# Performance work log

Measured on AMD Instinct MI355X. Metric: run time of the kernel, lower is better.

## Reference

```python
import jax, jax.numpy as jnp
import numpy as np

N, D, DFF, H, L = 98280, 192, 384, 8, 36
S = N // L  # 2730 sets per partition
HD = D // H
EPS = 1e-5


def _ln(x, g, b):
    m = x.mean(-1, keepdims=True)
    v = ((x - m) ** 2).mean(-1, keepdims=True)
    return (x - m) * jax.lax.rsqrt(v + EPS) * g + b


def _mha(q, k, v, Wqkv, bqkv, Wo, bo, mask):
    # q,k,v: (S, L, D); mask: (S, L), True = padded key
    Wq, Wk, Wv = jnp.split(Wqkv, 3, axis=0)
    bq, bk, bv = jnp.split(bqkv, 3)
    qh = (q @ Wq.T + bq).reshape(S, L, H, HD)
    kh = (k @ Wk.T + bk).reshape(S, L, H, HD)
    vh = (v @ Wv.T + bv).reshape(S, L, H, HD)
    scores = jnp.einsum('slhd,smhd->shlm', qh, kh) / np.sqrt(HD).astype(np.float32)
    scores = jnp.where(mask[:, None, None, :], -1e9, scores)
    attn = jax.nn.softmax(scores, axis=-1)
    out = jnp.einsum('shlm,smhd->slhd', attn, vh).reshape(S, L, D)
    return out @ Wo.T + bo


def _layer(x, pos, inds, mask, Wqkv, bqkv, Wo, bo, W1, b1, W2, b2,
           g1, be1, g2, be2, gn, bn):
    identity = x
    sf = x[inds]                 # gather voxels into sets: (S, L, D)
    qk = sf + pos[inds]          # pos added to q and k only (value = sf)
    src2 = _mha(qk, qk, sf, Wqkv, bqkv, Wo, bo, mask)
    flat = inds.reshape(-1)
    # torch.unique(return_inverse) + flip + scatter == take FIRST occurrence
    # of each voxel id; .at[].min is deterministic under duplicates.
    perm = jnp.full((N,), flat.shape[0], jnp.int32).at[flat].min(
        jnp.arange(flat.shape[0], dtype=jnp.int32))
    src2 = src2.reshape(-1, D)[perm]   # scatter back: (N, D)
    x = _ln(x + src2, g1, be1)
    ff = jnp.maximum(x @ W1.T + b1, 0.0) @ W2.T + b2
    x = _ln(x + ff, g2, be2)
    return _ln(x + identity, gn, bn)   # DSVT_EncoderLayer residual norm


def reference(src, inds0, inds1, mask0, mask1, pos0, pos1,
              Wqkv, bqkv, Wo, bo, W1, b1, W2, b2,
              g1, be1, g2, be2, gn, bn, block_id):
    inds = (inds0, inds1)
    masks = (mask0, mask1)
    pos = (pos0, pos1)
    out = src
    for i in range(2):  # two set partitions within the shift (shift_id = block_id % 2)
        out = _layer(out, pos[i], inds[i], masks[i],
                     Wqkv[i], bqkv[i], Wo[i], bo[i],
                     W1[i], b1[i], W2[i], b2[i],
                     g1[i], be1[i], g2[i], be2[i], gn[i], bn[i])
    return out


def setup_inputs():
    key = jax.random.key(0)
    ks = jax.random.split(key, 16)
    sd = 0.02
    return {
        "src": jax.random.normal(ks[0], (N, D), jnp.float32),
        "inds0": jax.random.permutation(ks[1], N).reshape(S, L).astype(jnp.int32),
        "inds1": jax.random.permutation(ks[2], N).reshape(S, L).astype(jnp.int32),
        "mask0": jnp.zeros((S, L), bool),
        "mask1": jnp.zeros((S, L), bool),
        "pos0": jax.random.normal(ks[3], (N, D), jnp.float32),
        "pos1": jax.random.normal(ks[4], (N, D), jnp.float32),
        "Wqkv": sd * jax.random.normal(ks[5], (2, 3 * D, D), jnp.float32),
        "bqkv": jnp.zeros((2, 3 * D), jnp.float32),
        "Wo": sd * jax.random.normal(ks[6], (2, D, D), jnp.float32),
        "bo": jnp.zeros((2, D), jnp.float32),
        "W1": sd * jax.random.normal(ks[7], (2, DFF, D), jnp.float32),
        "b1": jnp.zeros((2, DFF), jnp.float32),
        "W2": sd * jax.random.normal(ks[8], (2, D, DFF), jnp.float32),
        "b2": jnp.zeros((2, D), jnp.float32),
        "g1": jnp.ones((2, D), jnp.float32),
        "be1": jnp.zeros((2, D), jnp.float32),
        "g2": jnp.ones((2, D), jnp.float32),
        "be2": jnp.zeros((2, D), jnp.float32),
        "gn": jnp.ones((2, D), jnp.float32),
        "bn": jnp.zeros((2, D), jnp.float32),
        "block_id": 0,
    }
```

## Files before the change

### kernel.cpp

```cpp
#include <hip/hip_runtime.h>
#include <stdint.h>

#define NVOX   98280
#define S_SETS 2730
#define L_SET  36
#define D_MODEL 192
#define D_FF    384
#define N_HEADS 8
#define H_DIM   24

using s16x8 = __attribute__((ext_vector_type(8))) short;
using s16x4 = __attribute__((ext_vector_type(4))) short;
using f32x4 = __attribute__((ext_vector_type(4))) float;

__device__ __forceinline__ float bf2f(unsigned short h) {
    unsigned u = ((unsigned)h) << 16;
    return __builtin_bit_cast(float, u);
}
__device__ __forceinline__ unsigned short f2bf(float f) {
    unsigned u = __builtin_bit_cast(unsigned, f);
    u += 0x7FFF + ((u >> 16) & 1);
    return (unsigned short)(u >> 16);
}

__global__ __launch_bounds__(256)
void convert_f32_bf16(const float* __restrict__ src, short* __restrict__ dst, int n)
{
    int i = blockIdx.x * 256 + threadIdx.x;
    if (i < n) dst[i] = (short)f2bf(src[i]);
}

__global__ __launch_bounds__(256)
void gather_kernel(const float* __restrict__ x, const float* __restrict__ pos,
                   const int* __restrict__ inds,
                   short* __restrict__ qk, short* __restrict__ sf)
{
    int f = blockIdx.x * 4 + (threadIdx.x >> 6);
    int lane = threadIdx.x & 63;
    if (lane >= 48) return;
    int v = inds[f];
    float4 a = *(const float4*)(x + (size_t)v * D_MODEL + lane * 4);
    float4 p = *(const float4*)(pos + (size_t)v * D_MODEL + lane * 4);
    s16x4 q, s;
    q[0] = (short)f2bf(a.x + p.x); q[1] = (short)f2bf(a.y + p.y);
    q[2] = (short)f2bf(a.z + p.z); q[3] = (short)f2bf(a.w + p.w);
    s[0] = (short)f2bf(a.x); s[1] = (short)f2bf(a.y);
    s[2] = (short)f2bf(a.z); s[3] = (short)f2bf(a.w);
    *(s16x4*)(qk + (size_t)f * D_MODEL + lane * 4) = q;
    *(s16x4*)(sf + (size_t)f * D_MODEL + lane * 4) = s;
}

__global__ __launch_bounds__(512, 4)
void qkv_direct(const short* __restrict__ qk, const short* __restrict__ sf,
                const short* __restrict__ W, const float* __restrict__ bias,
                short* __restrict__ C, int n)
{
    __shared__ char Bs[36864];
    const int bx = blockIdx.x;
    const int sec = bx >> 1, half = bx & 1;
    const int colOff = sec * 192 + half * 96;
    const short* Ap = (sec == 2) ? sf : qk;
    const short* Wp = W + (size_t)colOff * 192;
    const int rowBase = blockIdx.y * 128;
    const int tid = threadIdx.x;

    #pragma unroll
    for (int t = tid; t < 2304; t += 512) {
        int row = t / 24, c8 = t % 24;
        s16x8 v = *(const s16x8*)(Wp + (size_t)row * 192 + c8 * 8);
        *(s16x8*)(Bs + row * 384 + ((c8 * 16) ^ ((row & 7) << 4))) = v;
    }
    __syncthreads();

    const int wid = tid >> 6, lane = tid & 63;
    const int lr = lane & 15, kb = lane >> 4;
    const int arow = rowBase + wid * 16 + lr;
    const bool rv = arow < n;
    const short* Arow = Ap + (size_t)arow * 192 + kb * 8;

    f32x4 acc[6] = {};
    #pragma unroll
    for (int ks = 0; ks < 6; ++ks) {
        s16x8 a = {};
        if (rv) a = *(const s16x8*)(Arow + ks * 32);
        s16x8 b[6];
        #pragma unroll
        for (int fj = 0; fj < 6; ++fj) {
            int row = fj * 16 + lr;
            b[fj] = *(const s16x8*)(Bs + row * 384 + ((ks * 64 + kb * 16) ^ ((row & 7) << 4)));
        }
        #pragma unroll
        for (int fj = 0; fj < 6; ++fj)
            acc[fj] = __builtin_amdgcn_mfma_f32_16x16x32_bf16(a, b[fj], acc[fj], 0, 0, 0);
    }
    #pragma unroll
    for (int fj = 0; fj < 6; ++fj) {
        int col = colOff + fj * 16 + lr;
        float bv = bias[col];
        #pragma unroll
        for (int r = 0; r < 4; ++r) {
            int grow = rowBase + wid * 16 + kb * 4 + r;
            if (grow < n)
                C[(size_t)grow * 576 + col] = (short)f2bf(acc[fj][r] + bv);
        }
    }
}

__global__ __launch_bounds__(512)
void attn_set_kernel(const short* __restrict__ qkv, const unsigned char* __restrict__ mask,
                     short* __restrict__ attn_out)
{
    const int s = blockIdx.x;
    __shared__ float KV[2][L_SET][200];
    __shared__ int msk[L_SET];
    const int tid = threadIdx.x;
    const int wid = tid >> 6;
    const int lane = tid & 63;

    for (int t = tid; t < 1728; t += 512) {
        int w = t >= 864;
        int u = t - (w ? 864 : 0);
        int l = u / 24, c8 = u % 24;
        s16x8 v = *(const s16x8*)(qkv + (size_t)(s * L_SET + l) * 576 + 192 + w * 192 + c8 * 8);
        #pragma unroll
        for (int e = 0; e < 8; ++e) KV[w][l][c8 * 8 + e] = bf2f((unsigned short)v[e]);
    }
    if (tid < L_SET) msk[tid] = mask[(size_t)s * L_SET + tid];
    __syncthreads();

    if (lane < L_SET) {
        float q[H_DIM];
        size_t qb = (size_t)(s * L_SET + lane) * 576 + wid * H_DIM;
        #pragma unroll
        for (int j = 0; j < 3; ++j) {
            s16x8 t8 = *(const s16x8*)(qkv + qb + j * 8);
            #pragma unroll
            for (int e = 0; e < 8; ++e) q[j * 8 + e] = bf2f((unsigned short)t8[e]);
        }
        float sc[L_SET];
        float mx = -1e30f;
        #pragma unroll
        for (int m = 0; m < L_SET; ++m) {
            float a = 0.f;
            #pragma unroll
            for (int j = 0; j < 6; ++j) {
                float4 k4 = *(const float4*)&KV[0][m][wid * H_DIM + j * 4];
                a = fmaf(q[j*4+0], k4.x, a); a = fmaf(q[j*4+1], k4.y, a);
                a = fmaf(q[j*4+2], k4.z, a); a = fmaf(q[j*4+3], k4.w, a);
            }
            a *= 0.20412414523193154f;
            if (msk[m] != 0) a = -1e9f;
            sc[m] = a;
            mx = fmaxf(mx, a);
        }
        float ssum = 0.f;
        #pragma unroll
        for (int m = 0; m < L_SET; ++m) { float e = __expf(sc[m] - mx); sc[m] = e; ssum += e; }
        const float rinv = 1.f / ssum;
        float o[H_DIM];
        #pragma unroll
        for (int d = 0; d < H_DIM; ++d) o[d] = 0.f;
        #pragma unroll
        for (int m = 0; m < L_SET; ++m) {
            float p = sc[m] * rinv;
            #pragma unroll
            for (int j = 0; j < 6; ++j) {
                float4 v4 = *(const float4*)&KV[1][m][wid * H_DIM + j * 4];
                o[j*4+0] = fmaf(p, v4.x, o[j*4+0]); o[j*4+1] = fmaf(p, v4.y, o[j*4+1]);
                o[j*4+2] = fmaf(p, v4.z, o[j*4+2]); o[j*4+3] = fmaf(p, v4.w, o[j*4+3]);
            }
        }
        size_t ob = (size_t)(s * L_SET + lane) * D_MODEL + wid * H_DIM;
        #pragma unroll
        for (int j = 0; j < 3; ++j) {
            s16x8 t8;
            #pragma unroll
            for (int e = 0; e < 8; ++e) t8[e] = (short)f2bf(o[j * 8 + e]);
            *(s16x8*)(attn_out + ob + j * 8) = t8;
        }
    }
}

__device__ __forceinline__ float wave_sum64(float v) {
    #pragma unroll
    for (int off = 32; off > 0; off >>= 1) v += __shfl_xor(v, off, 64);
    return v;
}

__global__ __launch_bounds__(512)
void wo_ln1(const short* __restrict__ attnb, const short* __restrict__ Wo,
            const float* __restrict__ bo, const int* __restrict__ inds,
            const float* __restrict__ xin,
            const float* __restrict__ g1, const float* __restrict__ be1,
            short* __restrict__ x1, int n)
{
    extern __shared__ char pool[];
    char* As = pool;
    char* Bs = pool + 49152;
    float* Cf = (float*)pool;
    const int rowBase = blockIdx.x * 128;
    const int tid = threadIdx.x;

    #pragma unroll
    for (int t = tid; t < 3072; t += 512) {
        int row = t / 24, c8 = t % 24;
        int grow = rowBase + row;
        s16x8 v = {};
        if (grow < n) v = *(const s16x8*)(attnb + (size_t)grow * 192 + c8 * 8);
        *(s16x8*)(As + row * 384 + ((c8 * 16) ^ ((row & 7) << 4))) = v;
    }
    #pragma unroll
    for (int t = tid; t < 4608; t += 512) {
        int row = t / 24, c8 = t % 24;
        s16x8 v = *(const s16x8*)(Wo + (size_t)row * 192 + c8 * 8);
        *(s16x8*)(Bs + row * 384 + ((c8 * 16) ^ ((row & 7) << 4))) = v;
    }
    __syncthreads();

    const int wid = tid >> 6, lane = tid & 63;
    const int lr = lane & 15, kb = lane >> 4;
    const int wm = wid & 3, wn = wid >> 2;
    f32x4 acc[2][6] = {};
    #pragma unroll
    for (int ks = 0; ks < 6; ++ks) {
        s16x8 a[2], b[6];
        #pragma unroll
        for (int fi = 0; fi < 2; ++fi) {
            int row = wm * 32 + fi * 16 + lr;
            a[fi] = *(const s16x8*)(As + row * 384 + ((ks * 64 + kb * 16) ^ ((row & 7) << 4)));
        }
        #pragma unroll
        for (int fj = 0; fj < 6; ++fj) {
            int row = wn * 96 + fj * 16 + lr;
            b[fj] = *(const s16x8*)(Bs + row * 384 + ((ks * 64 + kb * 16) ^ ((row & 7) << 4)));
        }
        #pragma unroll
        for (int fi = 0; fi < 2; ++fi)
            #pragma unroll
            for (int fj = 0; fj < 6; ++fj)
                acc[fi][fj] = __builtin_amdgcn_mfma_f32_16x16x32_bf16(a[fi], b[fj], acc[fi][fj], 0, 0, 0);
    }
    __syncthreads();
    #pragma unroll
    for (int fj = 0; fj < 6; ++fj) {
        int col = wn * 96 + fj * 16 + lr;
        float bv = bo[col];
        #pragma unroll
        for (int fi = 0; fi < 2; ++fi)
            #pragma unroll
            for (int r = 0; r < 4; ++r) {
                int row = wm * 32 + fi * 16 + kb * 4 + r;
                Cf[row * 192 + col] = acc[fi][fj][r] + bv;
            }
    }
    __syncthreads();

    int vv[16];
    #pragma unroll
    for (int i = 0; i < 16; ++i) {
        int f = rowBase + wid * 16 + i;
        vv[i] = (f < n) ? inds[f] : 0;
    }
    float4 xr[16];
    #pragma unroll
    for (int i = 0; i < 16; ++i)
        xr[i] = (lane < 48) ? *(const float4*)(xin + (size_t)vv[i] * D_MODEL + lane * 4)
                            : make_float4(0.f, 0.f, 0.f, 0.f);
    float4 gv = (lane < 48) ? *(const float4*)(g1 + lane * 4) : make_float4(0,0,0,0);
    float4 bv = (lane < 48) ? *(const float4*)(be1 + lane * 4) : make_float4(0,0,0,0);
    #pragma unroll
    for (int i = 0; i < 16; ++i) {
        int r = wid * 16 + i;
        int f = rowBase + r;
        float4 t = make_float4(0.f, 0.f, 0.f, 0.f);
        if (lane < 48) {
            float4 c4 = *(const float4*)&Cf[r * 192 + lane * 4];
            t.x = c4.x + xr[i].x; t.y = c4.y + xr[i].y;
            t.z = c4.z + xr[i].z; t.w = c4.w + xr[i].w;
        }
        float mean = wave_sum64(t.x + t.y + t.z + t.w) * (1.f / 192.f);
        float ss   = wave_sum64(t.x*t.x + t.y*t.y + t.z*t.z + t.w*t.w) * (1.f / 192.f);
        float inv = rsqrtf(ss - mean * mean + 1e-5f);
        if (lane < 48 && f < n) {
            s16x4 o;
            o[0] = (short)f2bf((t.x - mean) * inv * gv.x + bv.x);
            o[1] = (short)f2bf((t.y - mean) * inv * gv.y + bv.y);
            o[2] = (short)f2bf((t.z - mean) * inv * gv.z + bv.z);
            o[3] = (short)f2bf((t.w - mean) * inv * gv.w + bv.w);
            *(s16x4*)(x1 + (size_t)vv[i] * D_MODEL + lane * 4) = o;
        }
    }
}

__global__ __launch_bounds__(512)
void ffn_fused(const short* __restrict__ x1, const short* __restrict__ W1,
               const float* __restrict__ b1, const short* __restrict__ W2,
               const float* __restrict__ b2, const float* __restrict__ xin,
               const float* __restrict__ g2, const float* __restrict__ be2,
               const float* __restrict__ gn, const float* __restrict__ bn,
               float* __restrict__ outp, int n)
{
    extern __shared__ char pool[];
    char* Ax  = pool;
    char* W1c = pool + 49152;
    char* W2c = pool + 86016;
    char* Hc  = pool + 125952;
    float* Cf = (float*)(pool + 49152);
    const int rowBase = blockIdx.x * 128;
    const int tid = threadIdx.x;
    const int wid = tid >> 6, lane = tid & 63;
    const int lr = lane & 15, kb = lane >> 4;
    const int wm = wid & 3, wn = wid >> 2;

    #pragma unroll
    for (int t = tid; t < 3072; t += 512) {
        int row = t / 24, c8 = t % 24;
        int grow = rowBase + row;
        s16x8 v = {};
        if (grow < n) v = *(const s16x8*)(x1 + (size_t)grow * 192 + c8 * 8);
        *(s16x8*)(Ax + row * 384 + ((c8 * 16) ^ ((row & 7) << 4))) = v;
    }

    f32x4 acc2[2][6] = {};
    for (int c = 0; c < 4; ++c) {
        __syncthreads();
        #pragma unroll
        for (int t = tid; t < 2304; t += 512) {
            int row = t / 24, c8 = t % 24;
            s16x8 v = *(const s16x8*)(W1 + (size_t)(c * 96 + row) * 192 + c8 * 8);
            *(s16x8*)(W1c + row * 384 + ((c8 * 16) ^ ((row & 7) << 4))) = v;
        }
        #pragma unroll
        for (int t = tid; t < 2304; t += 512) {
            int row = t / 12, c8 = t % 12;
            s16x8 v = *(const s16x8*)(W2 + (size_t)row * 384 + c * 96 + c8 * 8);
            *(s16x8*)(W2c + row * 208 + c8 * 16) = v;
        }
        __syncthreads();
        f32x4 acc1[2][3] = {};
        #pragma unroll
        for (int ks = 0; ks < 6; ++ks) {
            s16x8 a[2], b[3];
            #pragma unroll
            for (int fi = 0; fi < 2; ++fi) {
                int row = wm * 32 + fi * 16 + lr;
                a[fi] = *(const s16x8*)(Ax + row * 384 + ((ks * 64 + kb * 16) ^ ((row & 7) << 4)));
            }
            #pragma unroll
            for (int fj = 0; fj < 3; ++fj) {
                int row = wn * 48 + fj * 16 + lr;
                b[fj] = *(const s16x8*)(W1c + row * 384 + ((ks * 64 + kb * 16) ^ ((row & 7) << 4)));
            }
            #pragma unroll
            for (int fi = 0; fi < 2; ++fi)
                #pragma unroll
                for (int fj = 0; fj < 3; ++fj)
                    acc1[fi][fj] = __builtin_amdgcn_mfma_f32_16x16x32_bf16(a[fi], b[fj], acc1[fi][fj], 0, 0, 0);
        }
        #pragma unroll
        for (int fj = 0; fj < 3; ++fj) {
            int col = wn * 48 + fj * 16 + lr;
            float b1v = b1[c * 96 + col];
            #pragma unroll
            for (int fi = 0; fi < 2; ++fi)
                #pragma unroll
                for (int r = 0; r < 4; ++r) {
                    int row = wm * 32 + fi * 16 + kb * 4 + r;
                    *(short*)(Hc + row * 208 + col * 2) =
                        (short)f2bf(fmaxf(acc1[fi][fj][r] + b1v, 0.f));
                }
        }
        __syncthreads();
        #pragma unroll
        for (int ks = 0; ks < 3; ++ks) {
            s16x8 a[2], b[6];
            #pragma unroll
            for (int fi = 0; fi < 2; ++fi) {
                int row = wm * 32 + fi * 16 + lr;
                a[fi] = *(const s16x8*)(Hc + row * 208 + ks * 64 + kb * 16);
            }
            #pragma unroll
            for (int fj = 0; fj < 6; ++fj) {
                int row = wn * 96 + fj * 16 + lr;
                b[fj] = *(const s16x8*)(W2c + row * 208 + ks * 64 + kb * 16);
            }
            #pragma unroll
            for (int fi = 0; fi < 2; ++fi)
                #pragma unroll
                for (int fj = 0; fj < 6; ++fj)
                    acc2[fi][fj] = __builtin_amdgcn_mfma_f32_16x16x32_bf16(a[fi], b[fj], acc2[fi][fj], 0, 0, 0);
        }
    }
    __syncthreads();
    #pragma unroll
    for (int fj = 0; fj < 6; ++fj) {
        int col = wn * 96 + fj * 16 + lr;
        float bv = b2[col];
        #pragma unroll
        for (int fi = 0; fi < 2; ++fi)
            #pragma unroll
            for (int r = 0; r < 4; ++r) {
                int row = wm * 32 + fi * 16 + kb * 4 + r;
                Cf[row * 192 + col] = acc2[fi][fj][r] + bv;
            }
    }
    __syncthreads();

    float4 xr[16];
    #pragma unroll
    for (int i = 0; i < 16; ++i) {
        int gvx = rowBase + wid * 16 + i;
        xr[i] = (lane < 48 && gvx < n)
              ? *(const float4*)(xin + (size_t)gvx * D_MODEL + lane * 4)
              : make_float4(0.f, 0.f, 0.f, 0.f);
    }
    float4 g2v = (lane < 48) ? *(const float4*)(g2 + lane * 4) : make_float4(0,0,0,0);
    float4 b2v = (lane < 48) ? *(const float4*)(be2 + lane * 4) : make_float4(0,0,0,0);
    float4 gnv = (lane < 48) ? *(const float4*)(gn + lane * 4) : make_float4(0,0,0,0);
    float4 bnv = (lane < 48) ? *(const float4*)(bn + lane * 4) : make_float4(0,0,0,0);
    #pragma unroll
    for (int i = 0; i < 16; ++i) {
        int r = wid * 16 + i;
        int gvx = rowBase + r;
        float4 t = make_float4(0.f, 0.f, 0.f, 0.f);
        if (lane < 48) {
            float4 f4 = *(const float4*)&Cf[r * 192 + lane * 4];
            int byteoff = r * 384 + (((lane >> 1) << 4) ^ ((r & 7) << 4)) + ((lane & 1) << 3);
            s16x4 xv = *(const s16x4*)(Ax + byteoff);
            t.x = f4.x + bf2f((unsigned short)xv[0]);
            t.y = f4.y + bf2f((unsigned short)xv[1]);
            t.z = f4.z + bf2f((unsigned short)xv[2]);
            t.w = f4.w + bf2f((unsigned short)xv[3]);
        }
        float m1 = wave_sum64(t.x + t.y + t.z + t.w) * (1.f / 192.f);
        float s1 = wave_sum64(t.x*t.x + t.y*t.y + t.z*t.z + t.w*t.w) * (1.f / 192.f);
        float i1 = rsqrtf(s1 - m1 * m1 + 1e-5f);
        float4 t2 = make_float4(0.f, 0.f, 0.f, 0.f);
        if (lane < 48) {
            t2.x = (t.x - m1) * i1 * g2v.x + b2v.x + xr[i].x;
            t2.y = (t.y - m1) * i1 * g2v.y + b2v.y + xr[i].y;
            t2.z = (t.z - m1) * i1 * g2v.z + b2v.z + xr[i].z;
            t2.w = (t.w - m1) * i1 * g2v.w + b2v.w + xr[i].w;
        }
        float m2 = wave_sum64(t2.x + t2.y + t2.z + t2.w) * (1.f / 192.f);
        float s2 = wave_sum64(t2.x*t2.x + t2.y*t2.y + t2.z*t2.z + t2.w*t2.w) * (1.f / 192.f);
        float i2 = rsqrtf(s2 - m2 * m2 + 1e-5f);
        if (lane < 48 && gvx < n) {
            float4 o;
            o.x = (t2.x - m2) * i2 * gnv.x + bnv.x;
            o.y = (t2.y - m2) * i2 * gnv.y + bnv.y;
            o.z = (t2.z - m2) * i2 * gnv.z + bnv.z;
            o.w = (t2.w - m2) * i2 * gnv.w + bnv.w;
            *(float4*)(outp + (size_t)gvx * D_MODEL + lane * 4) = o;
        }
    }
}

extern "C" void kernel_launch(void* const* d_in, const int* in_sizes, int n_in,
                              void* d_out, int out_size, void* d_ws, size_t ws_size,
                              hipStream_t stream)
{
    (void)in_sizes; (void)n_in; (void)out_size;
    const int N = NVOX;
    const float* src = (const float*)d_in[0];
    const int* inds[2] = {(const int*)d_in[1], (const int*)d_in[2]};
    const unsigned char* mask[2] = {(const unsigned char*)d_in[3], (const unsigned char*)d_in[4]};
    const float* pos[2] = {(const float*)d_in[5], (const float*)d_in[6]};
    const float* Wqkv = (const float*)d_in[7];
    const float* bqkv = (const float*)d_in[8];
    const float* Wo   = (const float*)d_in[9];
    const float* bo   = (const float*)d_in[10];
    const float* W1   = (const float*)d_in[11];
    const float* b1   = (const float*)d_in[12];
    const float* W2   = (const float*)d_in[13];
    const float* b2   = (const float*)d_in[14];
    const float* g1   = (const float*)d_in[15];
    const float* be1  = (const float*)d_in[16];
    const float* g2   = (const float*)d_in[17];
    const float* be2  = (const float*)d_in[18];
    const float* gn   = (const float*)d_in[19];
    const float* bn   = (const float*)d_in[20];

    float* out = (float*)d_out;
    short* wsS = (short*)d_ws;

    const size_t NE = (size_t)N * D_MODEL;
    short* wqkv_b = wsS;
    short* wo_b   = wsS + 221184;
    short* w1_b   = wsS + 294912;
    short* w2_b   = wsS + 442368;
    const size_t base = 1048576;
    short* qk    = wsS + base;
    short* sf    = qk + NE;
    short* qkvb  = sf + NE;
    short* attnb = qkvb + 3 * NE;
    short* x1    = attnb + NE;

    if (ws_size < (base + 7 * NE) * sizeof(short)) return;

    const dim3 blk(256);
    convert_f32_bf16<<<dim3(864), blk, 0, stream>>>(Wqkv, wqkv_b, 221184);
    convert_f32_bf16<<<dim3(288), blk, 0, stream>>>(Wo,   wo_b,   73728);
    convert_f32_bf16<<<dim3(576), blk, 0, stream>>>(W1,   w1_b,   147456);
    convert_f32_bf16<<<dim3(576), blk, 0, stream>>>(W2,   w2_b,   147456);

    const int RT = (N + 127) / 128;
    for (int i = 0; i < 2; ++i) {
        const float* xin = (i == 0) ? src : out;
        gather_kernel<<<dim3(24570), blk, 0, stream>>>(xin, pos[i], inds[i], qk, sf);
        qkv_direct<<<dim3(6, RT), dim3(512), 0, stream>>>(
            qk, sf, wqkv_b + (size_t)i * 110592, bqkv + i * 576, qkvb, N);
        attn_set_kernel<<<dim3(S_SETS), dim3(512), 0, stream>>>(qkvb, mask[i], attnb);
        wo_ln1<<<dim3(RT), dim3(512), 122880, stream>>>(
            attnb, wo_b + (size_t)i * 36864, bo + i * 192, inds[i], xin,
            g1 + i * 192, be1 + i * 192, x1, N);
        ffn_fused<<<dim3(RT), dim3(512), 152576, stream>>>(
            x1, w1_b + (size_t)i * 73728, b1 + i * 384, w2_b + (size_t)i * 73728,
            b2 + i * 192, xin, g2 + i * 192, be2 + i * 192,
            gn + i * 192, bn + i * 192, out, N);
    }
}
```

Baseline: 798.5 us.

## Split fused FFN into two direct GEMM kernels plus a separate double-LayerNorm kernel

Replaces the single fused FFN kernel, which kept the hidden activation in LDS and reloaded weight chunks per block, with two standalone GEMM kernels (FF1 with ReLU and FF2) that keep their whole weight slice resident in static shared memory and stream A rows straight from global memory. The final two LayerNorms move into a separate lightweight per-row kernel. The aim is higher occupancy and a simpler MFMA pipeline than the heavy 150KB-LDS fused kernel. In exchange the bf16 hidden tensor (N×384) and the FFN output now round-trip through global memory, adding HBM traffic and two extra launches per layer. The FFN output is also rounded to bf16 before the LayerNorm.

```diff
diff --git a/kernel.cpp b/kernel.cpp
--- a/kernel.cpp
+++ b/kernel.cpp
@@ -106,6 +106,110 @@
     }
 }
 
+__global__ __launch_bounds__(512, 4)
+void ff1_direct(const short* __restrict__ x1, const short* __restrict__ W1,
+                const float* __restrict__ b1, short* __restrict__ H, int n)
+{
+    __shared__ char Bs[36864];
+    const int colOff = blockIdx.x * 96;
+    const short* Wp = W1 + (size_t)colOff * 192;
+    const int rowBase = blockIdx.y * 128;
+    const int tid = threadIdx.x;
+
+    #pragma unroll
+    for (int t = tid; t < 2304; t += 512) {
+        int row = t / 24, c8 = t % 24;
+        s16x8 v = *(const s16x8*)(Wp + (size_t)row * 192 + c8 * 8);
+        *(s16x8*)(Bs + row * 384 + ((c8 * 16) ^ ((row & 7) << 4))) = v;
+    }
+    __syncthreads();
+
+    const int wid = tid >> 6, lane = tid & 63;
+    const int lr = lane & 15, kb = lane >> 4;
+    const int arow = rowBase + wid * 16 + lr;
+    const bool rv = arow < n;
+    const short* Arow = x1 + (size_t)arow * 192 + kb * 8;
+
+    f32x4 acc[6] = {};
+    #pragma unroll
+    for (int ks = 0; ks < 6; ++ks) {
+        s16x8 a = {};
+        if (rv) a = *(const s16x8*)(Arow + ks * 32);
+        s16x8 b[6];
+        #pragma unroll
+        for (int fj = 0; fj < 6; ++fj) {
+            int row = fj * 16 + lr;
+            b[fj] = *(const s16x8*)(Bs + row * 384 + ((ks * 64 + kb * 16) ^ ((row & 7) << 4)));
+        }
+        #pragma unroll
+        for (int fj = 0; fj < 6; ++fj)
+            acc[fj] = __builtin_amdgcn_mfma_f32_16x16x32_bf16(a, b[fj], acc[fj], 0, 0, 0);
+    }
+    #pragma unroll
+    for (int fj = 0; fj < 6; ++fj) {
+        int col = colOff + fj * 16 + lr;
+        float bv = b1[col];
+        #pragma unroll
+        for (int r = 0; r < 4; ++r) {
+            int grow = rowBase + wid * 16 + kb * 4 + r;
+            if (grow < n)
+                H[(size_t)grow * 384 + col] = (short)f2bf(fmaxf(acc[fj][r] + bv, 0.f));
+        }
+    }
+}
+
+__global__ __launch_bounds__(512, 2)
+void ff2_direct(const short* __restrict__ H, const short* __restrict__ W2,
+                const float* __restrict__ b2, short* __restrict__ f2, int n)
+{
+    __shared__ char Bs[73728];
+    const int colOff = blockIdx.x * 96;
+    const short* Wp = W2 + (size_t)colOff * 384;
+    const int rowBase = blockIdx.y * 128;
+    const int tid = threadIdx.x;
+
+    #pragma unroll
+    for (int t = tid; t < 4608; t += 512) {
+        int row = t / 48, c8 = t % 48;
+        s16x8 v = *(const s16x8*)(Wp + (size_t)row * 384 + c8 * 8);
+        *(s16x8*)(Bs + row * 768 + ((c8 * 16) ^ ((row & 7) << 4))) = v;
+    }
+    __syncthreads();
+
+    const int wid = tid >> 6, lane = tid & 63;
+    const int lr = lane & 15, kb = lane >> 4;
+    const int arow = rowBase + wid * 16 + lr;
+    const bool rv = arow < n;
+    const short* Arow = H + (size_t)arow * 384 + kb * 8;
+
+    f32x4 acc[6] = {};
+    #pragma unroll
+    for (int ks = 0; ks < 12; ++ks) {
+        s16x8 a = {};
+        if (rv) a = *(const s16x8*)(Arow + ks * 32);
+        s16x8 b[6];
+        #pragma unroll
+        for (int fj = 0; fj < 6; ++fj) {
+            int row = fj * 16 + lr;
+            b[fj] = *(const s16x8*)(Bs + row * 768 + ((ks * 64 + kb * 16) ^ ((row & 7) << 4)));
+        }
+        #pragma unroll
+        for (int fj = 0; fj < 6; ++fj)
+            acc[fj] = __builtin_amdgcn_mfma_f32_16x16x32_bf16(a, b[fj], acc[fj], 0, 0, 0);
+    }
+    #pragma unroll
+    for (int fj = 0; fj < 6; ++fj) {
+        int col = colOff + fj * 16 + lr;
+        float bv = b2[col];
+        #pragma unroll
+        for (int r = 0; r < 4; ++r) {
+            int grow = rowBase + wid * 16 + kb * 4 + r;
+            if (grow < n)
+                f2[(size_t)grow * 192 + col] = (short)f2bf(acc[fj][r] + bv);
+        }
+    }
+}
+
 __global__ __launch_bounds__(512)
 void attn_set_kernel(const short* __restrict__ qkv, const unsigned char* __restrict__ mask,
                      short* __restrict__ attn_out)
@@ -292,167 +396,50 @@
     }
 }
 
-__global__ __launch_bounds__(512)
-void ffn_fused(const short* __restrict__ x1, const short* __restrict__ W1,
-               const float* __restrict__ b1, const short* __restrict__ W2,
-               const float* __restrict__ b2, const float* __restrict__ xin,
-               const float* __restrict__ g2, const float* __restrict__ be2,
-               const float* __restrict__ gn, const float* __restrict__ bn,
-               float* __restrict__ outp, int n)
-{
-    extern __shared__ char pool[];
-    char* Ax  = pool;
-    char* W1c = pool + 49152;
-    char* W2c = pool + 86016;
-    char* Hc  = pool + 125952;
-    float* Cf = (float*)(pool + 49152);
-    const int rowBase = blockIdx.x * 128;
-    const int tid = threadIdx.x;
-    const int wid = tid >> 6, lane = tid & 63;
-    const int lr = lane & 15, kb = lane >> 4;
-    const int wm = wid & 3, wn = wid >> 2;
-
-    #pragma unroll
-    for (int t = tid; t < 3072; t += 512) {
-        int row = t / 24, c8 = t % 24;
-        int grow = rowBase + row;
-        s16x8 v = {};
-        if (grow < n) v = *(const s16x8*)(x1 + (size_t)grow * 192 + c8 * 8);
-        *(s16x8*)(Ax + row * 384 + ((c8 * 16) ^ ((row & 7) << 4))) = v;
-    }
-
-    f32x4 acc2[2][6] = {};
-    for (int c = 0; c < 4; ++c) {
-        __syncthreads();
-        #pragma unroll
-        for (int t = tid; t < 2304; t += 512) {
-            int row = t / 24, c8 = t % 24;
-            s16x8 v = *(const s16x8*)(W1 + (size_t)(c * 96 + row) * 192 + c8 * 8);
-            *(s16x8*)(W1c + row * 384 + ((c8 * 16) ^ ((row & 7) << 4))) = v;
-        }
-        #pragma unroll
-        for (int t = tid; t < 2304; t += 512) {
-            int row = t / 12, c8 = t % 12;
-            s16x8 v = *(const s16x8*)(W2 + (size_t)row * 384 + c * 96 + c8 * 8);
-            *(s16x8*)(W2c + row * 208 + c8 * 16) = v;
-        }
-        __syncthreads();
-        f32x4 acc1[2][3] = {};
-        #pragma unroll
-        for (int ks = 0; ks < 6; ++ks) {
-            s16x8 a[2], b[3];
-            #pragma unroll
-            for (int fi = 0; fi < 2; ++fi) {
-                int row = wm * 32 + fi * 16 + lr;
-                a[fi] = *(const s16x8*)(Ax + row * 384 + ((ks * 64 + kb * 16) ^ ((row & 7) << 4)));
-            }
-            #pragma unroll
-            for (int fj = 0; fj < 3; ++fj) {
-                int row = wn * 48 + fj * 16 + lr;
-                b[fj] = *(const s16x8*)(W1c + row * 384 + ((ks * 64 + kb * 16) ^ ((row & 7) << 4)));
-            }
-            #pragma unroll
-            for (int fi = 0; fi < 2; ++fi)
-                #pragma unroll
-                for (int fj = 0; fj < 3; ++fj)
-                    acc1[fi][fj] = __builtin_amdgcn_mfma_f32_16x16x32_bf16(a[fi], b[fj], acc1[fi][fj], 0, 0, 0);
-        }
-        #pragma unroll
-        for (int fj = 0; fj < 3; ++fj) {
-            int col = wn * 48 + fj * 16 + lr;
-            float b1v = b1[c * 96 + col];
-            #pragma unroll
-            for (int fi = 0; fi < 2; ++fi)
-                #pragma unroll
-                for (int r = 0; r < 4; ++r) {
-                    int row = wm * 32 + fi * 16 + kb * 4 + r;
-                    *(short*)(Hc + row * 208 + col * 2) =
-                        (short)f2bf(fmaxf(acc1[fi][fj][r] + b1v, 0.f));
-                }
-        }
-        __syncthreads();
-        #pragma unroll
-        for (int ks = 0; ks < 3; ++ks) {
-            s16x8 a[2], b[6];
-            #pragma unroll
-            for (int fi = 0; fi < 2; ++fi) {
-                int row = wm * 32 + fi * 16 + lr;
-                a[fi] = *(const s16x8*)(Hc + row * 208 + ks * 64 + kb * 16);
-            }
-            #pragma unroll
-            for (int fj = 0; fj < 6; ++fj) {
-                int row = wn * 96 + fj * 16 + lr;
-                b[fj] = *(const s16x8*)(W2c + row * 208 + ks * 64 + kb * 16);
-            }
-            #pragma unroll
-            for (int fi = 0; fi < 2; ++fi)
-                #pragma unroll
-                for (int fj = 0; fj < 6; ++fj)
-                    acc2[fi][fj] = __builtin_amdgcn_mfma_f32_16x16x32_bf16(a[fi], b[fj], acc2[fi][fj], 0, 0, 0);
-        }
-    }
-    __syncthreads();
-    #pragma unroll
-    for (int fj = 0; fj < 6; ++fj) {
-        int col = wn * 96 + fj * 16 + lr;
-        float bv = b2[col];
-        #pragma unroll
-        for (int fi = 0; fi < 2; ++fi)
-            #pragma unroll
-            for (int r = 0; r < 4; ++r) {
-                int row = wm * 32 + fi * 16 + kb * 4 + r;
-                Cf[row * 192 + col] = acc2[fi][fj][r] + bv;
-            }
-    }
-    __syncthreads();
-
-    float4 xr[16];
-    #pragma unroll
-    for (int i = 0; i < 16; ++i) {
-        int gvx = rowBase + wid * 16 + i;
-        xr[i] = (lane < 48 && gvx < n)
-              ? *(const float4*)(xin + (size_t)gvx * D_MODEL + lane * 4)
-              : make_float4(0.f, 0.f, 0.f, 0.f);
-    }
-    float4 g2v = (lane < 48) ? *(const float4*)(g2 + lane * 4) : make_float4(0,0,0,0);
-    float4 b2v = (lane < 48) ? *(const float4*)(be2 + lane * 4) : make_float4(0,0,0,0);
-    float4 gnv = (lane < 48) ? *(const float4*)(gn + lane * 4) : make_float4(0,0,0,0);
-    float4 bnv = (lane < 48) ? *(const float4*)(bn + lane * 4) : make_float4(0,0,0,0);
-    #pragma unroll
-    for (int i = 0; i < 16; ++i) {
-        int r = wid * 16 + i;
-        int gvx = rowBase + r;
-        float4 t = make_float4(0.f, 0.f, 0.f, 0.f);
-        if (lane < 48) {
-            float4 f4 = *(const float4*)&Cf[r * 192 + lane * 4];
-            int byteoff = r * 384 + (((lane >> 1) << 4) ^ ((r & 7) << 4)) + ((lane & 1) << 3);
-            s16x4 xv = *(const s16x4*)(Ax + byteoff);
-            t.x = f4.x + bf2f((unsigned short)xv[0]);
-            t.y = f4.y + bf2f((unsigned short)xv[1]);
-            t.z = f4.z + bf2f((unsigned short)xv[2]);
-            t.w = f4.w + bf2f((unsigned short)xv[3]);
-        }
-        float m1 = wave_sum64(t.x + t.y + t.z + t.w) * (1.f / 192.f);
-        float s1 = wave_sum64(t.x*t.x + t.y*t.y + t.z*t.z + t.w*t.w) * (1.f / 192.f);
-        float i1 = rsqrtf(s1 - m1 * m1 + 1e-5f);
-        float4 t2 = make_float4(0.f, 0.f, 0.f, 0.f);
-        if (lane < 48) {
-            t2.x = (t.x - m1) * i1 * g2v.x + b2v.x + xr[i].x;
-            t2.y = (t.y - m1) * i1 * g2v.y + b2v.y + xr[i].y;
-            t2.z = (t.z - m1) * i1 * g2v.z + b2v.z + xr[i].z;
-            t2.w = (t.w - m1) * i1 * g2v.w + b2v.w + xr[i].w;
-        }
-        float m2 = wave_sum64(t2.x + t2.y + t2.z + t2.w) * (1.f / 192.f);
-        float s2 = wave_sum64(t2.x*t2.x + t2.y*t2.y + t2.z*t2.z + t2.w*t2.w) * (1.f / 192.f);
-        float i2 = rsqrtf(s2 - m2 * m2 + 1e-5f);
-        if (lane < 48 && gvx < n) {
-            float4 o;
-            o.x = (t2.x - m2) * i2 * gnv.x + bnv.x;
-            o.y = (t2.y - m2) * i2 * gnv.y + bnv.y;
-            o.z = (t2.z - m2) * i2 * gnv.z + bnv.z;
-            o.w = (t2.w - m2) * i2 * gnv.w + bnv.w;
-            *(float4*)(outp + (size_t)gvx * D_MODEL + lane * 4) = o;
-        }
+__global__ __launch_bounds__(256)
+void ln_double_bf(const short* __restrict__ x1, const short* __restrict__ f2,
+                  const float* __restrict__ xin,
+                  const float* __restrict__ g2, const float* __restrict__ be2,
+                  const float* __restrict__ gn, const float* __restrict__ bn,
+                  float* __restrict__ outp)
+{
+    int v = blockIdx.x * 4 + (threadIdx.x >> 6);
+    int lane = threadIdx.x & 63;
+    float4 t   = make_float4(0.f, 0.f, 0.f, 0.f);
+    float4 idv = t, g2v = t, b2v = t, gnv = t, bnv = t;
+    if (lane < 48) {
+        s16x4 a = *(const s16x4*)(x1 + (size_t)v * D_MODEL + lane * 4);
+        s16x4 b = *(const s16x4*)(f2 + (size_t)v * D_MODEL + lane * 4);
+        idv = *(const float4*)(xin + (size_t)v * D_MODEL + lane * 4);
+        t.x = bf2f((unsigned short)a[0]) + bf2f((unsigned short)b[0]);
+        t.y = bf2f((unsigned short)a[1]) + bf2f((unsigned short)b[1]);
+        t.z = bf2f((unsigned short)a[2]) + bf2f((unsigned short)b[2]);
+        t.w = bf2f((unsigned short)a[3]) + bf2f((unsigned short)b[3]);
+        g2v = *(const float4*)(g2 + lane * 4);
+        b2v = *(const float4*)(be2 + lane * 4);
+        gnv = *(const float4*)(gn + lane * 4);
+        bnv = *(const float4*)(bn + lane * 4);
+    }
+    float m1 = wave_sum64(t.x + t.y + t.z + t.w) * (1.f / 192.f);
+    float s1 = wave_sum64(t.x*t.x + t.y*t.y + t.z*t.z + t.w*t.w) * (1.f / 192.f);
+    float i1 = rsqrtf(s1 - m1 * m1 + 1e-5f);
+    float4 t2 = make_float4(0.f, 0.f, 0.f, 0.f);
+    if (lane < 48) {
+        t2.x = (t.x - m1) * i1 * g2v.x + b2v.x + idv.x;
+        t2.y = (t.y - m1) * i1 * g2v.y + b2v.y + idv.y;
+        t2.z = (t.z - m1) * i1 * g2v.z + b2v.z + idv.z;
+        t2.w = (t.w - m1) * i1 * g2v.w + b2v.w + idv.w;
+    }
+    float m2 = wave_sum64(t2.x + t2.y + t2.z + t2.w) * (1.f / 192.f);
+    float s2 = wave_sum64(t2.x*t2.x + t2.y*t2.y + t2.z*t2.z + t2.w*t2.w) * (1.f / 192.f);
+    float i2 = rsqrtf(s2 - m2 * m2 + 1e-5f);
+    if (lane < 48) {
+        float4 o;
+        o.x = (t2.x - m2) * i2 * gnv.x + bnv.x;
+        o.y = (t2.y - m2) * i2 * gnv.y + bnv.y;
+        o.z = (t2.z - m2) * i2 * gnv.z + bnv.z;
+        o.w = (t2.w - m2) * i2 * gnv.w + bnv.w;
+        *(float4*)(outp + (size_t)v * D_MODEL + lane * 4) = o;
     }
 }
 
@@ -495,6 +482,8 @@
     short* qkvb  = sf + NE;
     short* attnb = qkvb + 3 * NE;
     short* x1    = attnb + NE;
+    short* hb    = qkvb;
+    short* f2    = qkvb + 2 * NE;
 
     if (ws_size < (base + 7 * NE) * sizeof(short)) return;
 
@@ -514,9 +503,11 @@
         wo_ln1<<<dim3(RT), dim3(512), 122880, stream>>>(
             attnb, wo_b + (size_t)i * 36864, bo + i * 192, inds[i], xin,
             g1 + i * 192, be1 + i * 192, x1, N);
-        ffn_fused<<<dim3(RT), dim3(512), 152576, stream>>>(
-            x1, w1_b + (size_t)i * 73728, b1 + i * 384, w2_b + (size_t)i * 73728,
-            b2 + i * 192, xin, g2 + i * 192, be2 + i * 192,
-            gn + i * 192, bn + i * 192, out, N);
-    }
-}
+        ff1_direct<<<dim3(4, RT), dim3(512), 0, stream>>>(
+            x1, w1_b + (size_t)i * 73728, b1 + i * 384, hb, N);
+        ff2_direct<<<dim3(2, RT), dim3(512), 0, stream>>>(
+            hb, w2_b + (size_t)i * 73728, b2 + i * 192, f2, N);
+        ln_double_bf<<<dim3(24570), blk, 0, stream>>>(
+            x1, f2, xin, g2 + i * 192, be2 + i * 192, gn + i * 192, bn + i * 192, out);
+    }
+}
```

Result: slower. 830.9 us (+4.1%).

## Compute per-set attention with MFMA, one wave per set and head

Applied to the files above, without the earlier changes.

Replaces the scalar-FMA attention kernel with one that launches a 64-thread block per (set, head). QK^T and PV are computed with bf16 16x16x32 MFMA tiles, padded from 36 to 48 rows. Softmax runs on the MFMA accumulators using 16-lane shuffle reductions, and probabilities and the transposed V are staged in XOR-swizzled LDS. This removes the old kernel's poor lane utilisation (only 36 of 64 lanes active) and its fp32 FMA-bound loops. In exchange, probabilities are rounded to bf16, extra padding work is done, and correctness relies on LDS ordering within a single wave with no explicit barrier.

```diff
diff --git a/kernel.cpp b/kernel.cpp
--- a/kernel.cpp
+++ b/kernel.cpp
@@ -106,77 +106,124 @@
     }
 }
 
-__global__ __launch_bounds__(512)
-void attn_set_kernel(const short* __restrict__ qkv, const unsigned char* __restrict__ mask,
-                     short* __restrict__ attn_out)
-{
-    const int s = blockIdx.x;
-    __shared__ float KV[2][L_SET][200];
-    __shared__ int msk[L_SET];
-    const int tid = threadIdx.x;
-    const int wid = tid >> 6;
-    const int lane = tid & 63;
-
-    for (int t = tid; t < 1728; t += 512) {
-        int w = t >= 864;
-        int u = t - (w ? 864 : 0);
-        int l = u / 24, c8 = u % 24;
-        s16x8 v = *(const s16x8*)(qkv + (size_t)(s * L_SET + l) * 576 + 192 + w * 192 + c8 * 8);
-        #pragma unroll
-        for (int e = 0; e < 8; ++e) KV[w][l][c8 * 8 + e] = bf2f((unsigned short)v[e]);
-    }
-    if (tid < L_SET) msk[tid] = mask[(size_t)s * L_SET + tid];
-    __syncthreads();
-
+__global__ __launch_bounds__(64)
+void attn_mfma(const short* __restrict__ qkv, const unsigned char* __restrict__ mask,
+               short* __restrict__ attn_out)
+{
+    const int s = blockIdx.x >> 3;
+    const int h = blockIdx.x & 7;
+    __shared__ short Pl[48 * 64];
+    __shared__ short Vt[32 * 64];
+    char* Pb = (char*)Pl;
+    char* Vb = (char*)Vt;
+    const int lane = threadIdx.x;
+    const int lr = lane & 15, g = lane >> 4;
+
+    #pragma unroll
+    for (int i = 0; i < 6; ++i)
+        *(s16x8*)(Pl + i * 512 + lane * 8) = (s16x8){};
+    #pragma unroll
+    for (int i = 0; i < 4; ++i)
+        *(s16x8*)(Vt + i * 512 + lane * 8) = (s16x8){};
     if (lane < L_SET) {
-        float q[H_DIM];
-        size_t qb = (size_t)(s * L_SET + lane) * 576 + wid * H_DIM;
+        const short* vrow = qkv + (size_t)(s * L_SET + lane) * 576 + 384 + h * H_DIM;
         #pragma unroll
         for (int j = 0; j < 3; ++j) {
-            s16x8 t8 = *(const s16x8*)(qkv + qb + j * 8);
-            #pragma unroll
-            for (int e = 0; e < 8; ++e) q[j * 8 + e] = bf2f((unsigned short)t8[e]);
-        }
-        float sc[L_SET];
-        float mx = -1e30f;
-        #pragma unroll
-        for (int m = 0; m < L_SET; ++m) {
-            float a = 0.f;
-            #pragma unroll
-            for (int j = 0; j < 6; ++j) {
-                float4 k4 = *(const float4*)&KV[0][m][wid * H_DIM + j * 4];
-                a = fmaf(q[j*4+0], k4.x, a); a = fmaf(q[j*4+1], k4.y, a);
-                a = fmaf(q[j*4+2], k4.z, a); a = fmaf(q[j*4+3], k4.w, a);
-            }
-            a *= 0.20412414523193154f;
-            if (msk[m] != 0) a = -1e9f;
-            sc[m] = a;
-            mx = fmaxf(mx, a);
-        }
-        float ssum = 0.f;
-        #pragma unroll
-        for (int m = 0; m < L_SET; ++m) { float e = __expf(sc[m] - mx); sc[m] = e; ssum += e; }
-        const float rinv = 1.f / ssum;
-        float o[H_DIM];
-        #pragma unroll
-        for (int d = 0; d < H_DIM; ++d) o[d] = 0.f;
-        #pragma unroll
-        for (int m = 0; m < L_SET; ++m) {
-            float p = sc[m] * rinv;
-            #pragma unroll
-            for (int j = 0; j < 6; ++j) {
-                float4 v4 = *(const float4*)&KV[1][m][wid * H_DIM + j * 4];
-                o[j*4+0] = fmaf(p, v4.x, o[j*4+0]); o[j*4+1] = fmaf(p, v4.y, o[j*4+1]);
-                o[j*4+2] = fmaf(p, v4.z, o[j*4+2]); o[j*4+3] = fmaf(p, v4.w, o[j*4+3]);
-            }
-        }
-        size_t ob = (size_t)(s * L_SET + lane) * D_MODEL + wid * H_DIM;
-        #pragma unroll
-        for (int j = 0; j < 3; ++j) {
-            s16x8 t8;
-            #pragma unroll
-            for (int e = 0; e < 8; ++e) t8[e] = (short)f2bf(o[j * 8 + e]);
-            *(s16x8*)(attn_out + ob + j * 8) = t8;
+            s16x8 v = *(const s16x8*)(vrow + j * 8);
+            #pragma unroll
+            for (int e = 0; e < 8; ++e) {
+                int d = j * 8 + e;
+                *(short*)(Vb + d * 128 + ((lane * 2) ^ ((d & 7) << 4))) = v[e];
+            }
+        }
+    }
+
+    s16x8 qa[3], kb[3];
+    #pragma unroll
+    for (int t = 0; t < 3; ++t) {
+        int rr = t * 16 + lr;
+        qa[t] = (s16x8){};
+        kb[t] = (s16x8){};
+        if (rr < L_SET && g < 3) {
+            const short* base = qkv + (size_t)(s * L_SET + rr) * 576 + h * H_DIM + g * 8;
+            qa[t] = *(const s16x8*)(base);
+            kb[t] = *(const s16x8*)(base + 192);
+        }
+    }
+    f32x4 sc[3][3] = {};
+    #pragma unroll
+    for (int mt = 0; mt < 3; ++mt)
+        #pragma unroll
+        for (int nt = 0; nt < 3; ++nt)
+            sc[mt][nt] = __builtin_amdgcn_mfma_f32_16x16x32_bf16(qa[mt], kb[nt], sc[mt][nt], 0, 0, 0);
+
+    const float scale = 0.20412414523193154f;
+    bool colmask[3];
+    #pragma unroll
+    for (int nt = 0; nt < 3; ++nt) {
+        int m = nt * 16 + lr;
+        colmask[nt] = (m >= L_SET) || (mask[(size_t)s * L_SET + (m < L_SET ? m : 0)] != 0);
+    }
+    #pragma unroll
+    for (int mt = 0; mt < 3; ++mt) {
+        #pragma unroll
+        for (int r = 0; r < 4; ++r) {
+            float v[3], ev[3];
+            #pragma unroll
+            for (int nt = 0; nt < 3; ++nt)
+                v[nt] = colmask[nt] ? -1e9f : sc[mt][nt][r] * scale;
+            float mx = fmaxf(fmaxf(v[0], v[1]), v[2]);
+            #pragma unroll
+            for (int off = 1; off < 16; off <<= 1) mx = fmaxf(mx, __shfl_xor(mx, off, 64));
+            float sm = 0.f;
+            #pragma unroll
+            for (int nt = 0; nt < 3; ++nt) { ev[nt] = __expf(v[nt] - mx); sm += ev[nt]; }
+            #pragma unroll
+            for (int off = 1; off < 16; off <<= 1) sm += __shfl_xor(sm, off, 64);
+            float rinv = 1.f / sm;
+            int q = mt * 16 + g * 4 + r;
+            #pragma unroll
+            for (int nt = 0; nt < 3; ++nt) {
+                int m = nt * 16 + lr;
+                *(short*)(Pb + q * 128 + ((m * 2) ^ ((q & 7) << 4))) =
+                    (short)f2bf(ev[nt] * rinv);
+            }
+        }
+    }
+
+    f32x4 o[3][2] = {};
+    #pragma unroll
+    for (int ks = 0; ks < 2; ++ks) {
+        s16x8 pa[3], vb[2];
+        #pragma unroll
+        for (int mt = 0; mt < 3; ++mt) {
+            int row = mt * 16 + lr;
+            pa[mt] = *(const s16x8*)(Pb + row * 128 + ((ks * 64 + g * 16) ^ ((row & 7) << 4)));
+        }
+        #pragma unroll
+        for (int nt = 0; nt < 2; ++nt) {
+            int row = nt * 16 + lr;
+            vb[nt] = *(const s16x8*)(Vb + row * 128 + ((ks * 64 + g * 16) ^ ((row & 7) << 4)));
+        }
+        #pragma unroll
+        for (int mt = 0; mt < 3; ++mt)
+            #pragma unroll
+            for (int nt = 0; nt < 2; ++nt)
+                o[mt][nt] = __builtin_amdgcn_mfma_f32_16x16x32_bf16(pa[mt], vb[nt], o[mt][nt], 0, 0, 0);
+    }
+
+    #pragma unroll
+    for (int mt = 0; mt < 3; ++mt) {
+        #pragma unroll
+        for (int nt = 0; nt < 2; ++nt) {
+            #pragma unroll
+            for (int r = 0; r < 4; ++r) {
+                int q = mt * 16 + g * 4 + r;
+                int d = nt * 16 + lr;
+                if (q < L_SET && d < H_DIM)
+                    attn_out[(size_t)(s * L_SET + q) * D_MODEL + h * H_DIM + d] =
+                        (short)f2bf(o[mt][nt][r]);
+            }
         }
     }
 }
@@ -510,7 +557,7 @@
         gather_kernel<<<dim3(24570), blk, 0, stream>>>(xin, pos[i], inds[i], qk, sf);
         qkv_direct<<<dim3(6, RT), dim3(512), 0, stream>>>(
             qk, sf, wqkv_b + (size_t)i * 110592, bqkv + i * 576, qkvb, N);
-        attn_set_kernel<<<dim3(S_SETS), dim3(512), 0, stream>>>(qkvb, mask[i], attnb);
+        attn_mfma<<<dim3(S_SETS * N_HEADS), dim3(64), 0, stream>>>(qkvb, mask[i], attnb);
         wo_ln1<<<dim3(RT), dim3(512), 122880, stream>>>(
             attnb, wo_b + (size_t)i * 36864, bo + i * 192, inds[i], xin,
             g1 + i * 192, be1 + i * 192, x1, N);
```

After: 790.1 us. Within noise of the previous version (-1.0%).
